# Performance work log

Measured on AMD Instinct MI355X. Metric: run time of the kernel, lower is better.

The kernel has to match this reference:

```python
import jax, jax.numpy as jnp
import numpy as np

# model dims (match init_kwargs)
D = 1024      # input_dim
H = 4096      # hidden_dim
O = 1024      # expert_output_dim
E = 8         # num_experts
K = 2         # top_k


def setup_inputs() -> dict:
    key = jax.random.key(0)
    ks = jax.random.split(key, 8)
    B, S = 2, 2048
    x = jax.random.normal(ks[0], (B, S, D), dtype=jnp.float32)
    s = 0.02
    Wr = jax.random.normal(ks[1], (D, E), dtype=jnp.float32) * s
    br = jnp.zeros((E,), dtype=jnp.float32)
    W1 = jax.random.normal(ks[2], (E, D, H), dtype=jnp.float32) * s
    b1 = jnp.zeros((E, H), dtype=jnp.float32)
    W2 = jax.random.normal(ks[3], (E, H, O), dtype=jnp.float32) * s
    b2 = jnp.zeros((E, O), dtype=jnp.float32)
    return {"x": x, "Wr": Wr, "br": br, "W1": W1, "b1": b1, "W2": W2, "b2": b2}


def reference(x, Wr, br, W1, b1, W2, b2):
    B, S, _ = x.shape
    T = B * S
    xf = x.reshape(T, D)                                  # [T, D]
    logits = xf @ Wr + br                                 # [T, E]
    topk_logits, topk_idx = jax.lax.top_k(logits, K)      # [T, K]
    gates = jax.nn.softmax(topk_logits, axis=1)           # softmax over the K selected logits
    # scatter gates into a dense [T, E] matrix (top-k indices are unique per token)
    dense_gates = jnp.zeros((T, E), dtype=logits.dtype).at[
        jnp.arange(T)[:, None], topk_idx
    ].set(gates)
    # run every expert FFN densely, then combine with (mostly-zero) gates
    h = jax.nn.relu(jnp.einsum('td,edh->teh', xf, W1) + b1)   # [T, E, H]
    y = jnp.einsum('teh,eho->teo', h, W2) + b2                # [T, E, O]
    out = jnp.einsum('te,teo->to', dense_gates, y)            # [T, O]
    return out.reshape(B, S, O)
```

## Files before the change

kernel.cpp:

```cpp
#include <hip/hip_runtime.h>
#include <stdint.h>

#define KD 1024
#define KH 4096
#define KO 1024
#define KE 8
#define KT 4096

typedef unsigned short u16;
typedef __bf16 bf16x8 __attribute__((ext_vector_type(8)));
typedef unsigned short ushort8 __attribute__((ext_vector_type(8)));
typedef float floatx4 __attribute__((ext_vector_type(4)));

__device__ __forceinline__ u16 f2bf(float f) {
  unsigned u = __float_as_uint(f);
  u += 0x7fffu + ((u >> 16) & 1u);
  return (u16)(u >> 16);
}

__device__ __forceinline__ void glds16(const u16* g, u16* l) {
  __builtin_amdgcn_global_load_lds(
      (const __attribute__((address_space(1))) unsigned int*)(g),
      (__attribute__((address_space(3))) unsigned int*)(l), 16, 0, 0);
}

__global__ void cvt_x_k(const float* __restrict__ x, u16* __restrict__ xbf) {
  int i = blockIdx.x * blockDim.x + threadIdx.x;
  float4 v = ((const float4*)x)[i];
  union { u16 u[4]; uint2 v2; } o;
  o.u[0] = f2bf(v.x); o.u[1] = f2bf(v.y); o.u[2] = f2bf(v.z); o.u[3] = f2bf(v.w);
  ((uint2*)xbf)[i] = o.v2;
}

__global__ __launch_bounds__(256) void transpose_k(const float* __restrict__ in,
                                                   u16* __restrict__ out, int R, int C) {
  __shared__ float tile[64][65];
  const int e = blockIdx.z;
  const float* I = in + (size_t)e * R * C;
  u16* Oo = out + (size_t)e * R * C;
  const int c0 = blockIdx.x * 64, r0 = blockIdx.y * 64;
  const int t = threadIdx.x;
  const int rr = t >> 4;
  const int c4 = (t & 15) << 2;
#pragma unroll
  for (int j = 0; j < 4; j++) {
    int r = rr + j * 16;
    float4 v = *(const float4*)&I[(size_t)(r0 + r) * C + c0 + c4];
    tile[r][c4] = v.x; tile[r][c4 + 1] = v.y; tile[r][c4 + 2] = v.z; tile[r][c4 + 3] = v.w;
  }
  __syncthreads();
  const int cc = t >> 3;
  const int rb = (t & 7) << 3;
#pragma unroll
  for (int j = 0; j < 2; j++) {
    int c = cc + j * 32;
    ushort8 o;
#pragma unroll
    for (int k = 0; k < 8; k++) o[k] = f2bf(tile[rb + k][c]);
    *(ushort8*)&Oo[(size_t)(c0 + c) * R + r0 + rb] = o;
  }
}

__global__ void router_k(const float* __restrict__ x, const float* __restrict__ Wr,
                         const float* __restrict__ br, int* __restrict__ eidx,
                         float2* __restrict__ gpair) {
  const int t = blockIdx.x;
  const int lane = threadIdx.x;
  const float* xr = x + (size_t)t * KD;
  double acc[KE];
#pragma unroll
  for (int e = 0; e < KE; e++) acc[e] = 0.0;
  for (int i = lane; i < KD; i += 64) {
    float xv = xr[i];
    const float* wr = Wr + i * KE;
#pragma unroll
    for (int e = 0; e < KE; e++) acc[e] += (double)xv * (double)wr[e];
  }
#pragma unroll
  for (int e = 0; e < KE; e++) {
#pragma unroll
    for (int m = 32; m > 0; m >>= 1) acc[e] += __shfl_xor(acc[e], m, 64);
  }
  if (lane == 0) {
    float l[KE];
#pragma unroll
    for (int e = 0; e < KE; e++) l[e] = (float)acc[e] + br[e];
    int i0 = 0;
#pragma unroll
    for (int e = 1; e < KE; e++) if (l[e] > l[i0]) i0 = e;
    int i1 = -1;
#pragma unroll
    for (int e = 0; e < KE; e++) {
      if (e == i0) continue;
      if (i1 < 0 || l[e] > l[i1]) i1 = e;
    }
    float g0 = 1.0f / (1.0f + expf(l[i1] - l[i0]));
    eidx[t] = i0 | (i1 << 4);
    gpair[t] = make_float2(g0, 1.0f - g0);
  }
}

__global__ __launch_bounds__(256) void bucket_k(const int* __restrict__ eidx,
                                                int* __restrict__ cnt,
                                                int* __restrict__ tok,
                                                int* __restrict__ pos) {
  const int e = blockIdx.x;
  const int tid = threadIdx.x;
  const int t0 = tid * 16;
  int f[16]; int c = 0;
#pragma unroll
  for (int j = 0; j < 16; j++) {
    int pk = eidx[t0 + j];
    int h0 = ((pk & 15) == e);
    int h1 = (((pk >> 4) & 15) == e);
    f[j] = h0 ? 1 : (h1 ? 2 : 0);
    c += (f[j] != 0);
  }
  __shared__ int sc[256];
  sc[tid] = c;
  __syncthreads();
  for (int d = 1; d < 256; d <<= 1) {
    int add = (tid >= d) ? sc[tid - d] : 0;
    __syncthreads();
    sc[tid] += add;
    __syncthreads();
  }
  int base = sc[tid] - c;
  if (tid == 0) cnt[e] = sc[255];
#pragma unroll
  for (int j = 0; j < 16; j++) {
    if (f[j]) {
      tok[(e << 12) + base] = t0 + j;
      pos[2 * (t0 + j) + (f[j] - 1)] = base;
      base++;
    }
  }
}

__global__ void offsets_k(const int* __restrict__ cnt, int* __restrict__ offs) {
  if (threadIdx.x == 0 && blockIdx.x == 0) {
    int s = 0;
#pragma unroll
    for (int e = 0; e < KE; e++) { offs[e] = s; s += cnt[e]; }
  }
}

__global__ __launch_bounds__(256) void gemm1_k(
    const u16* __restrict__ xbf, const u16* __restrict__ w1t,
    const float* __restrict__ b1, const int* __restrict__ cnt,
    const int* __restrict__ offs, const int* __restrict__ tok,
    u16* __restrict__ hbuf) {
  const int e = blockIdx.z;
  const int me = cnt[e];
  const int m0 = blockIdx.y * 128;
  if (m0 >= me) return;
  const int n0 = blockIdx.x * 128;
  const int oe = offs[e];
  const int* tk = tok + (e << 12);

  __shared__ u16 As[2 * 128 * 32];
  __shared__ u16 Bs[2 * 128 * 32];

  const int tid = threadIdx.x;
  const int lane = tid & 63;
  const int w = tid >> 6;
  const int wm = w >> 1, wn = w & 1;

  const int rr = lane >> 2;
  const int cc = (lane & 3) << 3;
  const int ar0 = m0 + w * 32 + rr;
  const int ar1 = ar0 + 16;
  const int ta0 = (ar0 < me) ? tk[ar0] : 0;
  const int ta1 = (ar1 < me) ? tk[ar1] : 0;
  const u16* ga0 = xbf + ((size_t)ta0 << 10) + cc;
  const u16* ga1 = xbf + ((size_t)ta1 << 10) + cc;
  const int br0 = n0 + w * 32 + rr;
  const u16* gb0 = w1t + ((size_t)e << 22) + ((size_t)br0 << 10) + cc;
  const u16* gb1 = gb0 + (16 << 10);
  u16* la00 = &As[w * 1024] + lane * 8;
  u16* la01 = la00 + 512;
  u16* la10 = la00 + 4096;
  u16* la11 = la00 + 4096 + 512;
  u16* lb00 = &Bs[w * 1024] + lane * 8;
  u16* lb01 = lb00 + 512;
  u16* lb10 = lb00 + 4096;
  u16* lb11 = lb00 + 4096 + 512;

  floatx4 acc[4][4] = {};
  const int fr = lane & 15;
  const int kq = (lane >> 4) << 3;

  for (int kt = 0; kt < KD / 64; ++kt) {
    const int k64 = kt * 64;
    __syncthreads();
    glds16(ga0 + k64,      la00);
    glds16(ga1 + k64,      la01);
    glds16(ga0 + k64 + 32, la10);
    glds16(ga1 + k64 + 32, la11);
    glds16(gb0 + k64,      lb00);
    glds16(gb1 + k64,      lb01);
    glds16(gb0 + k64 + 32, lb10);
    glds16(gb1 + k64 + 32, lb11);
    __builtin_amdgcn_s_waitcnt(0);
    __syncthreads();
#pragma unroll
    for (int p = 0; p < 2; p++) {
      bf16x8 af[4], bfr[4];
#pragma unroll
      for (int i = 0; i < 4; i++) {
        af[i]  = __builtin_bit_cast(bf16x8, *(const ushort8*)&As[p * 4096 + (wm * 64 + i * 16 + fr) * 32 + kq]);
        bfr[i] = __builtin_bit_cast(bf16x8, *(const ushort8*)&Bs[p * 4096 + (wn * 64 + i * 16 + fr) * 32 + kq]);
      }
#pragma unroll
      for (int mi = 0; mi < 4; mi++)
#pragma unroll
        for (int ni = 0; ni < 4; ni++)
          acc[mi][ni] = __builtin_amdgcn_mfma_f32_16x16x32_bf16(af[mi], bfr[ni], acc[mi][ni], 0, 0, 0);
    }
  }

  const int q = lane >> 4;
#pragma unroll
  for (int ni = 0; ni < 4; ni++) {
    const int gcol = n0 + wn * 64 + ni * 16 + fr;
    const float bb = b1[(e << 12) + gcol];
#pragma unroll
    for (int mi = 0; mi < 4; mi++) {
#pragma unroll
      for (int r = 0; r < 4; r++) {
        const int gr = m0 + wm * 64 + mi * 16 + q * 4 + r;
        if (gr < me) {
          float v = fmaxf(acc[mi][ni][r] + bb, 0.0f);
          hbuf[((size_t)(oe + gr) << 12) + gcol] = f2bf(v);
        }
      }
    }
  }
}

__global__ __launch_bounds__(256) void gemm2_k(
    const u16* __restrict__ hbuf, const u16* __restrict__ w2t,
    const int* __restrict__ cnt, const int* __restrict__ offs,
    float* __restrict__ y) {
  const int e = blockIdx.z;
  const int me = cnt[e];
  const int m0 = blockIdx.y * 128;
  if (m0 >= me) return;
  const int ks = blockIdx.x & 1;
  const int n0 = (blockIdx.x >> 1) * 128;
  const int k0 = ks * (KH / 2);
  const int oe = offs[e];

  __shared__ u16 As[2 * 128 * 32];
  __shared__ u16 Bs[2 * 128 * 32];

  const int tid = threadIdx.x;
  const int lane = tid & 63;
  const int w = tid >> 6;
  const int wm = w >> 1, wn = w & 1;

  const int rr = lane >> 2;
  const int cc = (lane & 3) << 3;
  const int ar0 = m0 + w * 32 + rr;
  const int ar1 = ar0 + 16;
  const int sl0 = oe + ((ar0 < me) ? ar0 : 0);
  const int sl1 = oe + ((ar1 < me) ? ar1 : 0);
  const u16* ga0 = hbuf + ((size_t)sl0 << 12) + k0 + cc;
  const u16* ga1 = hbuf + ((size_t)sl1 << 12) + k0 + cc;
  const int br0 = n0 + w * 32 + rr;
  const u16* gb0 = w2t + ((size_t)e << 22) + ((size_t)br0 << 12) + k0 + cc;
  const u16* gb1 = gb0 + (16 << 12);
  u16* la00 = &As[w * 1024] + lane * 8;
  u16* la01 = la00 + 512;
  u16* la10 = la00 + 4096;
  u16* la11 = la00 + 4096 + 512;
  u16* lb00 = &Bs[w * 1024] + lane * 8;
  u16* lb01 = lb00 + 512;
  u16* lb10 = lb00 + 4096;
  u16* lb11 = lb00 + 4096 + 512;

  floatx4 acc[4][4] = {};
  const int fr = lane & 15;
  const int kq = (lane >> 4) << 3;

  for (int kt = 0; kt < KH / 2 / 64; ++kt) {
    const int k64 = kt * 64;
    __syncthreads();
    glds16(ga0 + k64,      la00);
    glds16(ga1 + k64,      la01);
    glds16(ga0 + k64 + 32, la10);
    glds16(ga1 + k64 + 32, la11);
    glds16(gb0 + k64,      lb00);
    glds16(gb1 + k64,      lb01);
    glds16(gb0 + k64 + 32, lb10);
    glds16(gb1 + k64 + 32, lb11);
    __builtin_amdgcn_s_waitcnt(0);
    __syncthreads();
#pragma unroll
    for (int p = 0; p < 2; p++) {
      bf16x8 af[4], bfr[4];
#pragma unroll
      for (int i = 0; i < 4; i++) {
        af[i]  = __builtin_bit_cast(bf16x8, *(const ushort8*)&As[p * 4096 + (wm * 64 + i * 16 + fr) * 32 + kq]);
        bfr[i] = __builtin_bit_cast(bf16x8, *(const ushort8*)&Bs[p * 4096 + (wn * 64 + i * 16 + fr) * 32 + kq]);
      }
#pragma unroll
      for (int mi = 0; mi < 4; mi++)
#pragma unroll
        for (int ni = 0; ni < 4; ni++)
          acc[mi][ni] = __builtin_amdgcn_mfma_f32_16x16x32_bf16(af[mi], bfr[ni], acc[mi][ni], 0, 0, 0);
    }
  }

  const int q = lane >> 4;
  float* yk = y + ((size_t)ks << 23);
#pragma unroll
  for (int mi = 0; mi < 4; mi++) {
#pragma unroll
    for (int r = 0; r < 4; r++) {
      const int gr = m0 + wm * 64 + mi * 16 + q * 4 + r;
      if (gr < me) {
        float* yrow = yk + ((size_t)(oe + gr) << 10);
#pragma unroll
        for (int ni = 0; ni < 4; ni++)
          yrow[n0 + wn * 64 + ni * 16 + fr] = acc[mi][ni][r];
      }
    }
  }
}

__global__ __launch_bounds__(256) void combine_k(
    const float* __restrict__ y, const int* __restrict__ eidx,
    const float2* __restrict__ gp, const int* __restrict__ offs,
    const int* __restrict__ pos, const float* __restrict__ b2,
    float* __restrict__ out) {
  const int t = blockIdx.x;
  const int c4 = threadIdx.x << 2;
  const int pk = eidx[t];
  const int e0 = pk & 15, e1 = (pk >> 4) & 15;
  const float2 g = gp[t];
  const int s0 = offs[e0] + pos[2 * t];
  const int s1 = offs[e1] + pos[2 * t + 1];
  float4 a0 = *(const float4*)(y + ((size_t)s0 << 10) + c4);
  float4 a1 = *(const float4*)(y + (1ull << 23) + ((size_t)s0 << 10) + c4);
  float4 c0 = *(const float4*)(y + ((size_t)s1 << 10) + c4);
  float4 c1 = *(const float4*)(y + (1ull << 23) + ((size_t)s1 << 10) + c4);
  float4 ba = *(const float4*)(b2 + (e0 << 10) + c4);
  float4 bc = *(const float4*)(b2 + (e1 << 10) + c4);
  float4 o;
  o.x = g.x * (a0.x + a1.x + ba.x) + g.y * (c0.x + c1.x + bc.x);
  o.y = g.x * (a0.y + a1.y + ba.y) + g.y * (c0.y + c1.y + bc.y);
  o.z = g.x * (a0.z + a1.z + ba.z) + g.y * (c0.z + c1.z + bc.z);
  o.w = g.x * (a0.w + a1.w + ba.w) + g.y * (c0.w + c1.w + bc.w);
  *(float4*)(out + ((size_t)t << 10) + c4) = o;
}

extern "C" void kernel_launch(void* const* d_in, const int* in_sizes, int n_in,
                              void* d_out, int out_size, void* d_ws, size_t ws_size,
                              hipStream_t stream) {
  const float* x  = (const float*)d_in[0];
  const float* Wr = (const float*)d_in[1];
  const float* br = (const float*)d_in[2];
  const float* W1 = (const float*)d_in[3];
  const float* b1 = (const float*)d_in[4];
  const float* W2 = (const float*)d_in[5];
  const float* b2 = (const float*)d_in[6];
  float* out = (float*)d_out;

  char* ws = (char*)d_ws;
  size_t p = 0;
  auto alloc = [&](size_t bytes) {
    void* r = ws + p;
    p = (p + bytes + 255) & ~(size_t)255;
    return r;
  };
  int*    cnt   = (int*)alloc(KE * 4);
  int*    offs  = (int*)alloc(KE * 4);
  int*    eidx  = (int*)alloc((size_t)KT * 4);
  float2* gpair = (float2*)alloc((size_t)KT * 8);
  int*    pos   = (int*)alloc((size_t)2 * KT * 4);
  int*    tok   = (int*)alloc((size_t)KE * KT * 4);
  u16*    xbf   = (u16*)alloc((size_t)KT * KD * 2);
  u16*    w1t   = (u16*)alloc((size_t)KE * KD * KH * 2);
  u16*    w2t   = (u16*)alloc((size_t)KE * KH * KO * 2);
  u16*    hbuf  = (u16*)alloc((size_t)2 * KT * KH * 2);
  float*  y     = (float*)w1t;

  cvt_x_k<<<(KT * KD / 4) / 256, 256, 0, stream>>>(x, xbf);
  transpose_k<<<dim3(KH / 64, KD / 64, KE), 256, 0, stream>>>(W1, w1t, KD, KH);
  transpose_k<<<dim3(KO / 64, KH / 64, KE), 256, 0, stream>>>(W2, w2t, KH, KO);
  router_k<<<KT, 64, 0, stream>>>(x, Wr, br, eidx, gpair);
  bucket_k<<<KE, 256, 0, stream>>>(eidx, cnt, tok, pos);
  offsets_k<<<1, 64, 0, stream>>>(cnt, offs);
  gemm1_k<<<dim3(KH / 128, KT / 128, KE), 256, 0, stream>>>(xbf, w1t, b1, cnt, offs, tok, hbuf);
  gemm2_k<<<dim3(2 * KO / 128, KT / 128, KE), 256, 0, stream>>>(hbuf, w2t, cnt, offs, y);
  combine_k<<<KT, 256, 0, stream>>>(y, eidx, gpair, offs, pos, b2, out);
}
```

Measured before the change: 607.7 us.

## Double-buffer LDS tiles in both expert GEMMs with vmcnt-based prefetch pipelining

Both expert GEMM kernels now use two LDS buffers, so the global-to-LDS loads for the next 64-wide K tile are issued before computing on the current one. Partial vmcnt waits replace the full waitcnt-then-sync per iteration. The goal is to hide global memory latency behind the MFMA work. LDS use per block doubles to 64KB, which may reduce occupancy, and correctness now depends on the hand-placed waits and barriers.

```diff
diff --git a/kernel.cpp b/kernel.cpp
--- a/kernel.cpp
+++ b/kernel.cpp
@@ -23,6 +23,11 @@
       (const __attribute__((address_space(1))) unsigned int*)(g),
       (__attribute__((address_space(3))) unsigned int*)(l), 16, 0, 0);
 }
+
+#define WAITV8 asm volatile("s_waitcnt vmcnt(8)" ::: "memory")
+#define WAITV0 asm volatile("s_waitcnt vmcnt(0)" ::: "memory")
+#define WAITLG asm volatile("s_waitcnt lgkmcnt(0)" ::: "memory")
+#define BAR    __builtin_amdgcn_s_barrier()
 
 __global__ void cvt_x_k(const float* __restrict__ x, u16* __restrict__ xbf) {
   int i = blockIdx.x * blockDim.x + threadIdx.x;
@@ -158,8 +163,8 @@
   const int oe = offs[e];
   const int* tk = tok + (e << 12);
 
-  __shared__ u16 As[2 * 128 * 32];
-  __shared__ u16 Bs[2 * 128 * 32];
+  __shared__ u16 As[2 * 8192];
+  __shared__ u16 Bs[2 * 8192];
 
   const int tid = threadIdx.x;
   const int lane = tid & 63;
@@ -178,38 +183,30 @@
   const u16* gb0 = w1t + ((size_t)e << 22) + ((size_t)br0 << 10) + cc;
   const u16* gb1 = gb0 + (16 << 10);
   u16* la00 = &As[w * 1024] + lane * 8;
-  u16* la01 = la00 + 512;
-  u16* la10 = la00 + 4096;
-  u16* la11 = la00 + 4096 + 512;
   u16* lb00 = &Bs[w * 1024] + lane * 8;
-  u16* lb01 = lb00 + 512;
-  u16* lb10 = lb00 + 4096;
-  u16* lb11 = lb00 + 4096 + 512;
 
   floatx4 acc[4][4] = {};
   const int fr = lane & 15;
   const int kq = (lane >> 4) << 3;
 
-  for (int kt = 0; kt < KD / 64; ++kt) {
-    const int k64 = kt * 64;
-    __syncthreads();
-    glds16(ga0 + k64,      la00);
-    glds16(ga1 + k64,      la01);
-    glds16(ga0 + k64 + 32, la10);
-    glds16(ga1 + k64 + 32, la11);
-    glds16(gb0 + k64,      lb00);
-    glds16(gb1 + k64,      lb01);
-    glds16(gb0 + k64 + 32, lb10);
-    glds16(gb1 + k64 + 32, lb11);
-    __builtin_amdgcn_s_waitcnt(0);
-    __syncthreads();
+  auto stage = [&](int k64, int off) {
+    glds16(ga0 + k64,      la00 + off);
+    glds16(ga1 + k64,      la00 + off + 512);
+    glds16(ga0 + k64 + 32, la00 + off + 4096);
+    glds16(ga1 + k64 + 32, la00 + off + 4096 + 512);
+    glds16(gb0 + k64,      lb00 + off);
+    glds16(gb1 + k64,      lb00 + off + 512);
+    glds16(gb0 + k64 + 32, lb00 + off + 4096);
+    glds16(gb1 + k64 + 32, lb00 + off + 4096 + 512);
+  };
+  auto compute = [&](int off) {
 #pragma unroll
     for (int p = 0; p < 2; p++) {
       bf16x8 af[4], bfr[4];
 #pragma unroll
       for (int i = 0; i < 4; i++) {
-        af[i]  = __builtin_bit_cast(bf16x8, *(const ushort8*)&As[p * 4096 + (wm * 64 + i * 16 + fr) * 32 + kq]);
-        bfr[i] = __builtin_bit_cast(bf16x8, *(const ushort8*)&Bs[p * 4096 + (wn * 64 + i * 16 + fr) * 32 + kq]);
+        af[i]  = __builtin_bit_cast(bf16x8, *(const ushort8*)&As[off + p * 4096 + (wm * 64 + i * 16 + fr) * 32 + kq]);
+        bfr[i] = __builtin_bit_cast(bf16x8, *(const ushort8*)&Bs[off + p * 4096 + (wn * 64 + i * 16 + fr) * 32 + kq]);
       }
 #pragma unroll
       for (int mi = 0; mi < 4; mi++)
@@ -217,7 +214,16 @@
         for (int ni = 0; ni < 4; ni++)
           acc[mi][ni] = __builtin_amdgcn_mfma_f32_16x16x32_bf16(af[mi], bfr[ni], acc[mi][ni], 0, 0, 0);
     }
-  }
+  };
+
+  stage(0, 0);
+  stage(64, 8192);
+  for (int kt = 0; kt < KD / 64 - 2; kt += 2) {
+    WAITV8; BAR; compute(0);    WAITLG; BAR; stage((kt + 2) * 64, 0);
+    WAITV8; BAR; compute(8192); WAITLG; BAR; stage((kt + 3) * 64, 8192);
+  }
+  WAITV8; BAR; compute(0);
+  WAITV0; BAR; compute(8192);
 
   const int q = lane >> 4;
 #pragma unroll
@@ -251,8 +257,8 @@
   const int k0 = ks * (KH / 2);
   const int oe = offs[e];
 
-  __shared__ u16 As[2 * 128 * 32];
-  __shared__ u16 Bs[2 * 128 * 32];
+  __shared__ u16 As[2 * 8192];
+  __shared__ u16 Bs[2 * 8192];
 
   const int tid = threadIdx.x;
   const int lane = tid & 63;
@@ -271,38 +277,30 @@
   const u16* gb0 = w2t + ((size_t)e << 22) + ((size_t)br0 << 12) + k0 + cc;
   const u16* gb1 = gb0 + (16 << 12);
   u16* la00 = &As[w * 1024] + lane * 8;
-  u16* la01 = la00 + 512;
-  u16* la10 = la00 + 4096;
-  u16* la11 = la00 + 4096 + 512;
   u16* lb00 = &Bs[w * 1024] + lane * 8;
-  u16* lb01 = lb00 + 512;
-  u16* lb10 = lb00 + 4096;
-  u16* lb11 = lb00 + 4096 + 512;
 
   floatx4 acc[4][4] = {};
   const int fr = lane & 15;
   const int kq = (lane >> 4) << 3;
 
-  for (int kt = 0; kt < KH / 2 / 64; ++kt) {
-    const int k64 = kt * 64;
-    __syncthreads();
-    glds16(ga0 + k64,      la00);
-    glds16(ga1 + k64,      la01);
-    glds16(ga0 + k64 + 32, la10);
-    glds16(ga1 + k64 + 32, la11);
-    glds16(gb0 + k64,      lb00);
-    glds16(gb1 + k64,      lb01);
-    glds16(gb0 + k64 + 32, lb10);
-    glds16(gb1 + k64 + 32, lb11);
-    __builtin_amdgcn_s_waitcnt(0);
-    __syncthreads();
+  auto stage = [&](int k64, int off) {
+    glds16(ga0 + k64,      la00 + off);
+    glds16(ga1 + k64,      la00 + off + 512);
+    glds16(ga0 + k64 + 32, la00 + off + 4096);
+    glds16(ga1 + k64 + 32, la00 + off + 4096 + 512);
+    glds16(gb0 + k64,      lb00 + off);
+    glds16(gb1 + k64,      lb00 + off + 512);
+    glds16(gb0 + k64 + 32, lb00 + off + 4096);
+    glds16(gb1 + k64 + 32, lb00 + off + 4096 + 512);
+  };
+  auto compute = [&](int off) {
 #pragma unroll
     for (int p = 0; p < 2; p++) {
       bf16x8 af[4], bfr[4];
 #pragma unroll
       for (int i = 0; i < 4; i++) {
-        af[i]  = __builtin_bit_cast(bf16x8, *(const ushort8*)&As[p * 4096 + (wm * 64 + i * 16 + fr) * 32 + kq]);
-        bfr[i] = __builtin_bit_cast(bf16x8, *(const ushort8*)&Bs[p * 4096 + (wn * 64 + i * 16 + fr) * 32 + kq]);
+        af[i]  = __builtin_bit_cast(bf16x8, *(const ushort8*)&As[off + p * 4096 + (wm * 64 + i * 16 + fr) * 32 + kq]);
+        bfr[i] = __builtin_bit_cast(bf16x8, *(const ushort8*)&Bs[off + p * 4096 + (wn * 64 + i * 16 + fr) * 32 + kq]);
       }
 #pragma unroll
       for (int mi = 0; mi < 4; mi++)
@@ -310,7 +308,16 @@
         for (int ni = 0; ni < 4; ni++)
           acc[mi][ni] = __builtin_amdgcn_mfma_f32_16x16x32_bf16(af[mi], bfr[ni], acc[mi][ni], 0, 0, 0);
     }
-  }
+  };
+
+  stage(0, 0);
+  stage(64, 8192);
+  for (int kt = 0; kt < KH / 2 / 64 - 2; kt += 2) {
+    WAITV8; BAR; compute(0);    WAITLG; BAR; stage((kt + 2) * 64, 0);
+    WAITV8; BAR; compute(8192); WAITLG; BAR; stage((kt + 3) * 64, 8192);
+  }
+  WAITV8; BAR; compute(0);
+  WAITV0; BAR; compute(8192);
 
   const int q = lane >> 4;
   float* yk = y + ((size_t)ks << 23);
```

Result: no change. 614.6 us (+1.1%).
